# Kernel optimization log

Measured on AMD Instinct MI355X. Metric: run time of the kernel, lower is better.

Reference implementation:

```python
import jax, jax.numpy as jnp
import numpy as np

D_MODEL = 2048
N_HEADS = 16
N_KV_HEADS = 4
HEAD_DIM = D_MODEL // N_HEADS  # 128
WINDOW = 512
SOFTCAP = 50.0
ROPE_THETA = 10000.0
BATCH = 2
SEQ = 2048
NEG_INF = -1e30


def _rope_cos_sin(seq_len, head_dim, theta):
    # inv_freq over half the head dim, duplicated (HF rotate_half convention)
    inv_freq = 1.0 / (theta ** (jnp.arange(0, head_dim, 2, dtype=jnp.float32) / head_dim))
    freqs = jnp.arange(seq_len, dtype=jnp.float32)[:, None] * inv_freq[None, :]  # [S, hd/2]
    emb = jnp.concatenate([freqs, freqs], axis=-1)  # [S, hd]
    return jnp.cos(emb), jnp.sin(emb)


def _rotate_half(x):
    x1, x2 = jnp.split(x, 2, axis=-1)
    return jnp.concatenate([-x2, x1], axis=-1)


def _apply_rope(x, cos, sin):
    # x: [B, S, H, hd]; cos/sin: [S, hd] broadcast over batch & heads (unsqueeze_dim=2)
    c = cos[None, :, None, :]
    s = sin[None, :, None, :]
    return x * c + _rotate_half(x) * s


def setup_inputs() -> dict:
    key = jax.random.key(0)
    ks = jax.random.split(key, 5)
    scale_p = 1.0 / np.sqrt(D_MODEL)
    return {
        "hidden_states": jax.random.normal(ks[0], (BATCH, SEQ, D_MODEL), dtype=jnp.float32),
        "wq": jax.random.normal(ks[1], (N_HEADS * HEAD_DIM, D_MODEL), dtype=jnp.float32) * scale_p,
        "wk": jax.random.normal(ks[2], (N_KV_HEADS * HEAD_DIM, D_MODEL), dtype=jnp.float32) * scale_p,
        "wv": jax.random.normal(ks[3], (N_KV_HEADS * HEAD_DIM, D_MODEL), dtype=jnp.float32) * scale_p,
        "wo": jax.random.normal(ks[4], (D_MODEL, N_HEADS * HEAD_DIM), dtype=jnp.float32) * scale_p,
    }


def reference(hidden_states, wq, wk, wv, wo):
    B, S, _ = hidden_states.shape
    groups = N_HEADS // N_KV_HEADS
    scale = HEAD_DIM ** -0.5

    q = (hidden_states @ wq.T).reshape(B, S, N_HEADS, HEAD_DIM)
    k = (hidden_states @ wk.T).reshape(B, S, N_KV_HEADS, HEAD_DIM)
    v = (hidden_states @ wv.T).reshape(B, S, N_KV_HEADS, HEAD_DIM)

    cos, sin = _rope_cos_sin(S, HEAD_DIM, ROPE_THETA)
    q = _apply_rope(q, cos, sin)
    k = _apply_rope(k, cos, sin)

    # GQA head expansion: each kv head serves `groups` query heads
    k = jnp.repeat(k, groups, axis=2)  # [B, S, H, hd]
    v = jnp.repeat(v, groups, axis=2)

    scores = jnp.einsum("bqhd,bkhd->bhqk", q, k) * scale
    scores = SOFTCAP * jnp.tanh(scores / SOFTCAP)

    i = jnp.arange(S)[:, None]
    j = jnp.arange(S)[None, :]
    allowed = (j <= i) & (j > i - WINDOW)  # causal + sliding window
    scores = jnp.where(allowed[None, None], scores, NEG_INF)

    attn = jax.nn.softmax(scores, axis=-1)
    out = jnp.einsum("bhqk,bkhd->bqhd", attn, v).reshape(B, S, N_HEADS * HEAD_DIM)
    return out @ wo.T
```

## Files before the change

kernel.cpp:

```cpp
#include <hip/hip_runtime.h>
#include <hip/hip_bf16.h>
#include <stdint.h>

#define DM    2048
#define NH    16
#define NKVH  4
#define HD    128
#define WIN   512
#define SEQL  2048
#define BAT   2
#define MR    (BAT*SEQL)
#define NQKV  3072
#define QKSCALE 0.08838834764831845f
#define CAP   50.0f
#define C1F (QKSCALE * 2.0f * 1.4426950408889634f / CAP)
#define C2F (-144.26950408889634f)

typedef unsigned short u16;
typedef __attribute__((ext_vector_type(8))) short short8;
typedef __attribute__((ext_vector_type(4))) float f32x4;
typedef __attribute__((ext_vector_type(16))) float f32x16;

__device__ __forceinline__ u16 f2bf(float f) {
  union { float f; uint32_t u; } v; v.f = f;
  uint32_t r = v.u + 0x7FFFu + ((v.u >> 16) & 1u);
  return (u16)(r >> 16);
}
__device__ __forceinline__ float bf2f(u16 h) {
  union { uint32_t u; float f; } v; v.u = ((uint32_t)h) << 16; return v.f;
}
__device__ __forceinline__ void gld16(const void* g, void* l) {
  __builtin_amdgcn_global_load_lds((const __attribute__((address_space(1))) void*)g,
                                   (__attribute__((address_space(3))) void*)l,
                                   16, 0, 0);
}
__device__ __forceinline__ float exp_softcap(float sv) {
  float t = __builtin_amdgcn_exp2f(sv);
  float u = __builtin_amdgcn_rcpf(t + 1.0f);
  return __builtin_amdgcn_exp2f(u * C2F);
}

__global__ void k_cast(const float* __restrict__ src, u16* __restrict__ dst, int n4) {
  int i = blockIdx.x * 256 + threadIdx.x;
  if (i >= n4) return;
  float4 v = ((const float4*)src)[i];
  ushort4 o;
  o.x = f2bf(v.x); o.y = f2bf(v.y); o.z = f2bf(v.z); o.w = f2bf(v.w);
  ((ushort4*)dst)[i] = o;
}

__global__ void k_rope_table(float* __restrict__ c, float* __restrict__ sn) {
  int s = blockIdx.x, i = threadIdx.x;
  float invf = expf(-(float)i * (9.210340371976184f / 64.0f));
  float a = (float)s * invf;
  c[(s << 6) + i]  = cosf(a);
  sn[(s << 6) + i] = sinf(a);
}

template <typename OutT>
__global__ __launch_bounds__(256, 3) void k_gemm_bt(const u16* __restrict__ A,
                                                    const u16* __restrict__ Bm,
                                                    OutT* __restrict__ C,
                                                    int N, int K) {
  __shared__ __align__(16) u16 ldsA[128 * 64];
  __shared__ __align__(16) u16 ldsB[128 * 64];
  const int t = threadIdx.x;

  const int nwg  = gridDim.x * gridDim.y;
  const int flat = blockIdx.y * gridDim.x + blockIdx.x;
  const int cpx  = nwg >> 3;
  const int swz  = (flat & 7) * cpx + (flat >> 3);
  const int bn = swz % gridDim.x, bm = swz / gridDim.x;

  const int m0 = bm * 128, n0 = bn * 128;
  const int lane = t & 63, wid = t >> 6;
  const int lr = lane & 15, lk = lane >> 4;
  const int wr = (wid >> 1) * 64, wc = (wid & 1) * 64;
  const int nt = K >> 6;

  const int srow = t >> 3;
  const int scol = (((t & 7) ^ (srow & 7)) << 3);

  f32x4 acc[4][4];
  #pragma unroll
  for (int mi = 0; mi < 4; ++mi)
    #pragma unroll
    for (int ni = 0; ni < 4; ++ni) acc[mi][ni] = f32x4{0.f, 0.f, 0.f, 0.f};

  for (int kt = 0; kt < nt; ++kt) {
    {
      const u16* a0 = A  + (size_t)(m0 + srow) * K + kt * 64 + scol;
      const u16* b0 = Bm + (size_t)(n0 + srow) * K + kt * 64 + scol;
      #pragma unroll
      for (int i = 0; i < 4; ++i) {
        gld16(a0 + (size_t)(i * 32) * K, &ldsA[i * 2048 + t * 8]);
        gld16(b0 + (size_t)(i * 32) * K, &ldsB[i * 2048 + t * 8]);
      }
    }
    __syncthreads();
    #pragma unroll
    for (int ks = 0; ks < 2; ++ks) {
      const int c = ks * 4 + lk;
      short8 af[4], bfv[4];
      #pragma unroll
      for (int mi = 0; mi < 4; ++mi) {
        const int ra = wr + mi * 16 + lr;
        af[mi] = *(const short8*)(ldsA + ra * 64 + ((c ^ (ra & 7)) << 3));
      }
      #pragma unroll
      for (int ni = 0; ni < 4; ++ni) {
        const int rb = wc + ni * 16 + lr;
        bfv[ni] = *(const short8*)(ldsB + rb * 64 + ((c ^ (rb & 7)) << 3));
      }
      #pragma unroll
      for (int mi = 0; mi < 4; ++mi)
        #pragma unroll
        for (int ni = 0; ni < 4; ++ni)
          acc[mi][ni] = __builtin_amdgcn_mfma_f32_16x16x32_bf16(af[mi], bfv[ni], acc[mi][ni], 0, 0, 0);
    }
    if (kt + 1 < nt) __syncthreads();
  }

  #pragma unroll
  for (int mi = 0; mi < 4; ++mi) {
    #pragma unroll
    for (int ni = 0; ni < 4; ++ni) {
      const int r0 = m0 + wr + mi * 16 + lk * 4;
      const int c  = n0 + wc + ni * 16 + lr;
      #pragma unroll
      for (int r = 0; r < 4; ++r) {
        float v = acc[mi][ni][r];
        if constexpr (__is_same(OutT, float)) C[(size_t)(r0 + r) * N + c] = v;
        else                                  C[(size_t)(r0 + r) * N + c] = f2bf(v);
      }
    }
  }
}

__global__ void k_rope_q(const u16* __restrict__ C, const float* __restrict__ cosT,
                         const float* __restrict__ sinT, u16* __restrict__ qr) {
  int idx = blockIdx.x * 256 + threadIdx.x;
  int i = idx & 63, hh = (idx >> 6) & 15, m = idx >> 10;
  int s = m & (SEQL - 1), b = m >> 11;
  size_t cb = (size_t)m * NQKV + hh * HD + i;
  float x1 = bf2f(C[cb]), x2 = bf2f(C[cb + 64]);
  float c = cosT[(s << 6) + i], sn = sinT[(s << 6) + i];
  size_t ob = ((size_t)(b * NH + hh) * SEQL + s) * HD + i;
  qr[ob]      = f2bf((x1 * c - x2 * sn) * C1F);
  qr[ob + 64] = f2bf((x2 * c + x1 * sn) * C1F);
}

__global__ void k_rope_k(const u16* __restrict__ C, const float* __restrict__ cosT,
                         const float* __restrict__ sinT, u16* __restrict__ kr) {
  int idx = blockIdx.x * 256 + threadIdx.x;
  int i = idx & 63, kvh = (idx >> 6) & 3, m = idx >> 8;
  int s = m & (SEQL - 1), b = m >> 11;
  size_t cb = (size_t)m * NQKV + 2048 + kvh * HD + i;
  float x1 = bf2f(C[cb]), x2 = bf2f(C[cb + 64]);
  float c = cosT[(s << 6) + i], sn = sinT[(s << 6) + i];
  size_t ob = ((size_t)(b * NKVH + kvh) * SEQL + s) * HD + i;
  kr[ob]      = f2bf(x1 * c - x2 * sn);
  kr[ob + 64] = f2bf(x2 * c + x1 * sn);
}

__global__ void k_vt(const u16* __restrict__ C, u16* __restrict__ vt) {
  int idx = blockIdx.x * 256 + threadIdx.x;
  int s = idx & (SEQL - 1);
  int d = (idx >> 11) & 127;
  int kvh = (idx >> 18) & 3;
  int b = idx >> 20;
  int m = b * SEQL + s;
  vt[idx] = C[(size_t)m * NQKV + 2560 + kvh * HD + d];
}

__global__ __launch_bounds__(256, 2) void k_attn(const u16* __restrict__ qr,
                                                 const u16* __restrict__ kr,
                                                 const u16* __restrict__ vt,
                                                 u16* __restrict__ ao) {
  __shared__ __align__(16) u16 kbuf[2][32 * 128];
  __shared__ __align__(16) u16 vbuf[2][128 * 32];

  const int t = threadIdx.x;
  const int wid = t >> 6, lane = t & 63;
  const int l31 = lane & 31, lh = lane >> 5;
  const int h = blockIdx.x, bq = blockIdx.y, b = blockIdx.z;
  const int kvh = h >> 2;
  const int Q0 = bq * 128;
  const int q0w = Q0 + wid * 32;
  const u16* qb = qr + (size_t)(b * NH + h) * SEQL * HD;
  const u16* kb = kr + (size_t)(b * NKVH + kvh) * SEQL * HD;
  const u16* vb = vt + (size_t)(b * NKVH + kvh) * HD * SEQL;

  short8 qf[8];
  #pragma unroll
  for (int ks = 0; ks < 8; ++ks)
    qf[ks] = *(const short8*)(qb + (size_t)(q0w + l31) * HD + ks * 16 + lh * 8);

  f32x16 o[4];
  #pragma unroll
  for (int dt = 0; dt < 4; ++dt)
    #pragma unroll
    for (int i = 0; i < 16; ++i) o[dt][i] = 0.f;
  float lsum = 0.f;

  int lo = Q0 - (WIN - 1); if (lo < 0) lo = 0;
  const int ktlo = lo >> 5, kthi = (Q0 + 127) >> 5;

  auto stageK = [&](int bufi, int kv0) {
    #pragma unroll
    for (int i = 0; i < 2; ++i) {
      int c = t + i * 256;
      int bb = c << 4;
      int sb = bb ^ (((bb >> 8) & 7) << 4);
      gld16(kb + (size_t)(kv0 + (sb >> 8)) * HD + ((sb & 255) >> 1),
            &kbuf[bufi][c << 3]);
    }
  };
  auto stageV = [&](int bufi, int kv0) {
    #pragma unroll
    for (int i = 0; i < 2; ++i) {
      int c = t + i * 256;
      int bb = c << 4;
      int sb = bb ^ (((bb >> 7) & 3) << 4);
      gld16(vb + (size_t)(sb >> 6) * SEQL + kv0 + ((sb & 63) >> 1),
            &vbuf[bufi][c << 3]);
    }
  };

  stageK(0, ktlo << 5);
  stageV(0, ktlo << 5);
  __syncthreads();

  for (int kt = ktlo; kt <= kthi; ++kt) {
    const int cur = kt & 1;
    if (kt < kthi) { stageK(cur ^ 1, (kt + 1) << 5); stageV(cur ^ 1, (kt + 1) << 5); }
    const int kv0 = kt << 5;
    if (kv0 + 31 >= q0w - (WIN - 1) && kv0 <= q0w + 31) {
      f32x16 sv;
      #pragma unroll
      for (int i = 0; i < 16; ++i) sv[i] = 0.f;
      const u16* lks = kbuf[cur];
      #pragma unroll
      for (int ks = 0; ks < 8; ++ks) {
        int bo = (l31 * 256 + ks * 32 + lh * 16) ^ ((l31 & 7) << 4);
        short8 kf = *(const short8*)(lks + (bo >> 1));
        sv = __builtin_amdgcn_mfma_f32_32x32x16_bf16(kf, qf[ks], sv, 0, 0, 0);
      }
      float p[16];
      const bool interior = (kv0 + 31 <= q0w) && (kv0 >= q0w + 32 - WIN);
      if (interior) {
        #pragma unroll
        for (int r = 0; r < 16; ++r) p[r] = exp_softcap(sv[r]);
      } else {
        const int qg = q0w + l31;
        #pragma unroll
        for (int r = 0; r < 16; ++r) {
          const int kg = kv0 + (r & 3) + 8 * (r >> 2) + 4 * lh;
          float e = exp_softcap(sv[r]);
          p[r] = (kg <= qg && kg > qg - WIN) ? e : 0.f;
        }
      }
      #pragma unroll
      for (int r = 0; r < 16; ++r) lsum += p[r];

      uint32_t w[8];
      #pragma unroll
      for (int r2 = 0; r2 < 8; ++r2) {
        __hip_bfloat162 u = __float22bfloat162_rn(float2{p[2 * r2], p[2 * r2 + 1]});
        w[r2] = *(uint32_t*)&u;
      }
      uint32_t z0 = lh ? w[0] : w[2], z1 = lh ? w[1] : w[3];
      uint32_t z2 = lh ? w[4] : w[6], z3 = lh ? w[5] : w[7];
      uint32_t x0 = __shfl_xor((int)z0, 32), x1 = __shfl_xor((int)z1, 32);
      uint32_t x2 = __shfl_xor((int)z2, 32), x3 = __shfl_xor((int)z3, 32);
      union U8 { uint32_t u[4]; short8 s; };
      U8 pa0, pa1;
      pa0.u[0] = lh ? x0 : w[0];  pa0.u[1] = lh ? x1 : w[1];
      pa0.u[2] = lh ? w[2] : x0;  pa0.u[3] = lh ? w[3] : x1;
      pa1.u[0] = lh ? x2 : w[4];  pa1.u[1] = lh ? x3 : w[5];
      pa1.u[2] = lh ? w[6] : x2;  pa1.u[3] = lh ? w[7] : x3;

      const u16* lvs = vbuf[cur];
      #pragma unroll
      for (int ks2 = 0; ks2 < 2; ++ks2) {
        const short8 paf = ks2 ? pa1.s : pa0.s;
        #pragma unroll
        for (int dt = 0; dt < 4; ++dt) {
          int row = dt * 32 + l31;
          int bo = (row * 64 + ks2 * 32 + lh * 16) ^ (((row >> 1) & 3) << 4);
          short8 vf = *(const short8*)(lvs + (bo >> 1));
          o[dt] = __builtin_amdgcn_mfma_f32_32x32x16_bf16(paf, vf, o[dt], 0, 0, 0);
        }
      }
    }
    __syncthreads();
  }

  lsum += __shfl_xor(lsum, 32);
  float linv = 1.0f / lsum;
  #pragma unroll
  for (int rr = 0; rr < 4; ++rr) {
    #pragma unroll
    for (int r = 0; r < 4; ++r) {
      const int crow = r + 8 * rr + 4 * lh;
      float inv = __shfl(linv, crow);
      const int srow = q0w + crow;
      u16* op = ao + (size_t)(b * SEQL + srow) * DM + h * HD;
      #pragma unroll
      for (int dt = 0; dt < 4; ++dt)
        op[dt * 32 + l31] = f2bf(o[dt][rr * 4 + r] * inv);
    }
  }
}

extern "C" void kernel_launch(void* const* d_in, const int* in_sizes, int n_in,
                              void* d_out, int out_size, void* d_ws, size_t ws_size,
                              hipStream_t stream) {
  (void)in_sizes; (void)n_in; (void)out_size; (void)ws_size;
  const float* hs = (const float*)d_in[0];
  const float* wq = (const float*)d_in[1];
  const float* wk = (const float*)d_in[2];
  const float* wv = (const float*)d_in[3];
  const float* wo = (const float*)d_in[4];
  float* out = (float*)d_out;

  u16* ws    = (u16*)d_ws;
  u16* A_bf  = ws;
  u16* Wqkv  = A_bf + 8388608;
  u16* Cqkv  = Wqkv + 6291456;
  u16* q_r   = Cqkv + 12582912;
  u16* k_r   = q_r + 8388608;
  u16* vTb   = k_r + 2097152;
  float* cosT = (float*)(vTb + 2097152);
  float* sinT = cosT + 131072;
  u16* Wo   = Cqkv;
  u16* aout = A_bf;

  k_cast<<<8192, 256, 0, stream>>>(hs, A_bf, 2097152);
  k_cast<<<4096, 256, 0, stream>>>(wq, Wqkv, 1048576);
  k_cast<<<1024, 256, 0, stream>>>(wk, Wqkv + 4194304, 262144);
  k_cast<<<1024, 256, 0, stream>>>(wv, Wqkv + 5242880, 262144);
  k_rope_table<<<2048, 64, 0, stream>>>(cosT, sinT);

  k_gemm_bt<u16><<<dim3(NQKV / 128, MR / 128), 256, 0, stream>>>(A_bf, Wqkv, Cqkv, NQKV, DM);

  k_rope_q<<<16384, 256, 0, stream>>>(Cqkv, cosT, sinT, q_r);
  k_rope_k<<<4096, 256, 0, stream>>>(Cqkv, cosT, sinT, k_r);
  k_vt<<<8192, 256, 0, stream>>>(Cqkv, vTb);
  k_cast<<<4096, 256, 0, stream>>>(wo, Wo, 1048576);

  k_attn<<<dim3(NH, SEQL / 128, BAT), 256, 0, stream>>>(q_r, k_r, vTb, aout);

  k_gemm_bt<float><<<dim3(DM / 128, MR / 128), 256, 0, stream>>>(aout, Wo, out, DM, DM);
}
```

Before: 189.9 us.

## Fuse RoPE and V transpose into the QKV GEMM epilogue

Adds a dedicated QKV GEMM whose epilogue applies RoPE to the Q and K tiles, swapping rotate-half partners between waves through LDS, and writes V directly in transposed layout. This removes the intermediate Cqkv buffer along with the three separate rope_q, rope_k and vt kernels and their global round-trips. In exchange the epilogue gains extra LDS syncs, cos/sin table loads and scattered 2-byte stores. The Wo cast moves earlier because its workspace no longer aliases Cqkv.

```diff
diff --git a/kernel.cpp b/kernel.cpp
--- a/kernel.cpp
+++ b/kernel.cpp
@@ -57,6 +57,132 @@
   sn[(s << 6) + i] = sinf(a);
 }
 
+__global__ __launch_bounds__(256, 3) void k_gemm_qkv(const u16* __restrict__ A,
+                                                     const u16* __restrict__ Bm,
+                                                     u16* __restrict__ qrout,
+                                                     u16* __restrict__ krout,
+                                                     u16* __restrict__ vtout,
+                                                     const float* __restrict__ cosT,
+                                                     const float* __restrict__ sinT) {
+  __shared__ __align__(16) u16 ldsbuf[2 * 128 * 64];
+  u16* ldsA = ldsbuf;
+  u16* ldsB = ldsbuf + 128 * 64;
+  const int t = threadIdx.x;
+  const int K = DM;
+
+  const int nwg  = gridDim.x * gridDim.y;
+  const int flat = blockIdx.y * gridDim.x + blockIdx.x;
+  const int cpx  = nwg >> 3;
+  const int swz  = (flat & 7) * cpx + (flat >> 3);
+  const int bn = swz % gridDim.x, bm = swz / gridDim.x;
+
+  const int m0 = bm * 128, n0 = bn * 128;
+  const int lane = t & 63, wid = t >> 6;
+  const int lr = lane & 15, lk = lane >> 4;
+  const int wr = (wid >> 1) * 64, wc = (wid & 1) * 64;
+  const int nt = K >> 6;
+
+  const int srow = t >> 3;
+  const int scol = (((t & 7) ^ (srow & 7)) << 3);
+
+  f32x4 acc[4][4];
+  #pragma unroll
+  for (int mi = 0; mi < 4; ++mi)
+    #pragma unroll
+    for (int ni = 0; ni < 4; ++ni) acc[mi][ni] = f32x4{0.f, 0.f, 0.f, 0.f};
+
+  for (int kt = 0; kt < nt; ++kt) {
+    {
+      const u16* a0 = A  + (size_t)(m0 + srow) * K + kt * 64 + scol;
+      const u16* b0 = Bm + (size_t)(n0 + srow) * K + kt * 64 + scol;
+      #pragma unroll
+      for (int i = 0; i < 4; ++i) {
+        gld16(a0 + (size_t)(i * 32) * K, &ldsA[i * 2048 + t * 8]);
+        gld16(b0 + (size_t)(i * 32) * K, &ldsB[i * 2048 + t * 8]);
+      }
+    }
+    __syncthreads();
+    #pragma unroll
+    for (int ks = 0; ks < 2; ++ks) {
+      const int c = ks * 4 + lk;
+      short8 af[4], bfv[4];
+      #pragma unroll
+      for (int mi = 0; mi < 4; ++mi) {
+        const int ra = wr + mi * 16 + lr;
+        af[mi] = *(const short8*)(ldsA + ra * 64 + ((c ^ (ra & 7)) << 3));
+      }
+      #pragma unroll
+      for (int ni = 0; ni < 4; ++ni) {
+        const int rb = wc + ni * 16 + lr;
+        bfv[ni] = *(const short8*)(ldsB + rb * 64 + ((c ^ (rb & 7)) << 3));
+      }
+      #pragma unroll
+      for (int mi = 0; mi < 4; ++mi)
+        #pragma unroll
+        for (int ni = 0; ni < 4; ++ni)
+          acc[mi][ni] = __builtin_amdgcn_mfma_f32_16x16x32_bf16(af[mi], bfv[ni], acc[mi][ni], 0, 0, 0);
+    }
+    if (kt + 1 < nt) __syncthreads();
+  }
+
+  __syncthreads();
+  const int bb2 = m0 >> 11;
+
+  if (bn < 20) {
+    float* exch = (float*)ldsbuf;
+    const bool isq = (bn < 16);
+    u16* obase = isq ? (qrout + (size_t)(bb2 * NH + bn) * SEQL * HD)
+                     : (krout + (size_t)(bb2 * NKVH + (bn - 16)) * SEQL * HD);
+    #pragma unroll
+    for (int half = 0; half < 2; ++half) {
+      #pragma unroll
+      for (int mi2 = 0; mi2 < 2; ++mi2)
+        #pragma unroll
+        for (int ni = 0; ni < 4; ++ni)
+          #pragma unroll
+          for (int r = 0; r < 4; ++r)
+            exch[(wid * 32 + mi2 * 16 + ni * 4 + r) * 64 + lane] = acc[half * 2 + mi2][ni][r];
+      __syncthreads();
+      #pragma unroll
+      for (int mi2 = 0; mi2 < 2; ++mi2) {
+        const int mi = half * 2 + mi2;
+        const int rbase = m0 + wr + mi * 16 + lk * 4;
+        #pragma unroll
+        for (int ni = 0; ni < 4; ++ni) {
+          const int d64 = ni * 16 + lr;
+          const int d   = wc + d64;
+          #pragma unroll
+          for (int r = 0; r < 4; ++r) {
+            const int s = (rbase + r) & (SEQL - 1);
+            float x = acc[mi][ni][r];
+            float y = exch[((wid ^ 1) * 32 + mi2 * 16 + ni * 4 + r) * 64 + lane];
+            float cc = cosT[(s << 6) + d64], ss = sinT[(s << 6) + d64];
+            float ov = (wc == 0) ? (x * cc - y * ss) : (x * cc + y * ss);
+            if (isq) ov *= C1F;
+            obase[(size_t)s * HD + d] = f2bf(ov);
+          }
+        }
+      }
+      __syncthreads();
+    }
+  } else {
+    const int kvh = bn - 20;
+    u16* vb = vtout + (size_t)(bb2 * NKVH + kvh) * HD * SEQL;
+    #pragma unroll
+    for (int mi = 0; mi < 4; ++mi) {
+      const int s0 = (m0 + wr + mi * 16 + lk * 4) & (SEQL - 1);
+      #pragma unroll
+      for (int ni = 0; ni < 4; ++ni) {
+        const int d = wc + ni * 16 + lr;
+        ushort4 w4;
+        w4.x = f2bf(acc[mi][ni][0]); w4.y = f2bf(acc[mi][ni][1]);
+        w4.z = f2bf(acc[mi][ni][2]); w4.w = f2bf(acc[mi][ni][3]);
+        *(ushort4*)(vb + (size_t)d * SEQL + s0) = w4;
+      }
+    }
+  }
+}
+
 template <typename OutT>
 __global__ __launch_bounds__(256, 3) void k_gemm_bt(const u16* __restrict__ A,
                                                     const u16* __restrict__ Bm,
@@ -135,42 +261,6 @@
       }
     }
   }
-}
-
-__global__ void k_rope_q(const u16* __restrict__ C, const float* __restrict__ cosT,
-                         const float* __restrict__ sinT, u16* __restrict__ qr) {
-  int idx = blockIdx.x * 256 + threadIdx.x;
-  int i = idx & 63, hh = (idx >> 6) & 15, m = idx >> 10;
-  int s = m & (SEQL - 1), b = m >> 11;
-  size_t cb = (size_t)m * NQKV + hh * HD + i;
-  float x1 = bf2f(C[cb]), x2 = bf2f(C[cb + 64]);
-  float c = cosT[(s << 6) + i], sn = sinT[(s << 6) + i];
-  size_t ob = ((size_t)(b * NH + hh) * SEQL + s) * HD + i;
-  qr[ob]      = f2bf((x1 * c - x2 * sn) * C1F);
-  qr[ob + 64] = f2bf((x2 * c + x1 * sn) * C1F);
-}
-
-__global__ void k_rope_k(const u16* __restrict__ C, const float* __restrict__ cosT,
-                         const float* __restrict__ sinT, u16* __restrict__ kr) {
-  int idx = blockIdx.x * 256 + threadIdx.x;
-  int i = idx & 63, kvh = (idx >> 6) & 3, m = idx >> 8;
-  int s = m & (SEQL - 1), b = m >> 11;
-  size_t cb = (size_t)m * NQKV + 2048 + kvh * HD + i;
-  float x1 = bf2f(C[cb]), x2 = bf2f(C[cb + 64]);
-  float c = cosT[(s << 6) + i], sn = sinT[(s << 6) + i];
-  size_t ob = ((size_t)(b * NKVH + kvh) * SEQL + s) * HD + i;
-  kr[ob]      = f2bf(x1 * c - x2 * sn);
-  kr[ob + 64] = f2bf(x2 * c + x1 * sn);
-}
-
-__global__ void k_vt(const u16* __restrict__ C, u16* __restrict__ vt) {
-  int idx = blockIdx.x * 256 + threadIdx.x;
-  int s = idx & (SEQL - 1);
-  int d = (idx >> 11) & 127;
-  int kvh = (idx >> 18) & 3;
-  int b = idx >> 20;
-  int m = b * SEQL + s;
-  vt[idx] = C[(size_t)m * NQKV + 2560 + kvh * HD + d];
 }
 
 __global__ __launch_bounds__(256, 2) void k_attn(const u16* __restrict__ qr,
@@ -327,27 +417,23 @@
   u16* ws    = (u16*)d_ws;
   u16* A_bf  = ws;
   u16* Wqkv  = A_bf + 8388608;
-  u16* Cqkv  = Wqkv + 6291456;
-  u16* q_r   = Cqkv + 12582912;
+  u16* Wo    = Wqkv + 6291456;
+  u16* q_r   = Wo + 4194304;
   u16* k_r   = q_r + 8388608;
   u16* vTb   = k_r + 2097152;
   float* cosT = (float*)(vTb + 2097152);
   float* sinT = cosT + 131072;
-  u16* Wo   = Cqkv;
   u16* aout = A_bf;
 
   k_cast<<<8192, 256, 0, stream>>>(hs, A_bf, 2097152);
   k_cast<<<4096, 256, 0, stream>>>(wq, Wqkv, 1048576);
   k_cast<<<1024, 256, 0, stream>>>(wk, Wqkv + 4194304, 262144);
   k_cast<<<1024, 256, 0, stream>>>(wv, Wqkv + 5242880, 262144);
+  k_cast<<<4096, 256, 0, stream>>>(wo, Wo, 1048576);
   k_rope_table<<<2048, 64, 0, stream>>>(cosT, sinT);
 
-  k_gemm_bt<u16><<<dim3(NQKV / 128, MR / 128), 256, 0, stream>>>(A_bf, Wqkv, Cqkv, NQKV, DM);
-
-  k_rope_q<<<16384, 256, 0, stream>>>(Cqkv, cosT, sinT, q_r);
-  k_rope_k<<<4096, 256, 0, stream>>>(Cqkv, cosT, sinT, k_r);
-  k_vt<<<8192, 256, 0, stream>>>(Cqkv, vTb);
-  k_cast<<<4096, 256, 0, stream>>>(wo, Wo, 1048576);
+  k_gemm_qkv<<<dim3(NQKV / 128, MR / 128), 256, 0, stream>>>(A_bf, Wqkv, q_r, k_r, vTb,
+                                                             cosT, sinT);
 
   k_attn<<<dim3(NH, SEQL / 128, BAT), 256, 0, stream>>>(q_r, k_r, vTb, aout);
 
```

Result: faster. 175.7 us (-7.5%).
